# Optimization experiments

Hardware: AMD Instinct MI355X
Metric: run time of the kernel (lower is better)

The kernel has to match this reference:

```python
import jax, jax.numpy as jnp
import numpy as np

B, T, V, H = 256, 2048, 128, 64  # batch, seq_len, vocab/input_size, hidden_size


def setup_inputs() -> dict:
    key = jax.random.key(0)
    ks = jax.random.split(key, 11)
    s = 0.1  # weight scale
    d = jnp.float32
    return {
        "x": jax.random.normal(ks[0], (B, T, V), dtype=d),
        "W_f": jax.random.normal(ks[1], (V + H, H), dtype=d) * s,
        "b_f": jax.random.normal(ks[2], (H,), dtype=d) * s,
        "W_if": jax.random.normal(ks[3], (V + H, H), dtype=d) * s,
        "b_if": jax.random.normal(ks[4], (H,), dtype=d) * s,
        "W_ic": jax.random.normal(ks[5], (V + H, H), dtype=d) * s,
        "b_ic": jax.random.normal(ks[6], (H,), dtype=d) * s,
        "W_o": jax.random.normal(ks[7], (V + H, H), dtype=d) * s,
        "b_o": jax.random.normal(ks[8], (H,), dtype=d) * s,
        "W_out": jax.random.normal(ks[9], (H, V), dtype=d) * s,
        "b_out": jax.random.normal(ks[10], (V,), dtype=d) * s,
    }


def reference(x, W_f, b_f, W_if, b_if, W_ic, b_ic, W_o, b_o, W_out, b_out):
    # Manual LSTM cell from the source, stepped over time with lax.scan.
    # Per step (faithful to forward()+getOut()):
    #   s = concat(x_t, h);  f = sigmoid(s@W_f+b_f);  c = c*f
    #   add = tanh(s@W_ic+b_ic); af = sigmoid(s@W_if+b_if); c = c + add*af
    #   o = sigmoid(s@W_o+b_o);  h = tanh(c)*o
    #   out = softmax(h@W_out+b_out)
    b, t = x.shape[0], x.shape[1]
    h0 = jnp.zeros((b, W_f.shape[1]), dtype=x.dtype)
    c0 = jnp.zeros_like(h0)

    def step(carry, x_t):
        h, c = carry
        s = jnp.concatenate([x_t, h], axis=1)          # [B, V+H]
        f = jax.nn.sigmoid(s @ W_f + b_f)
        add = jnp.tanh(s @ W_ic + b_ic)
        af = jax.nn.sigmoid(s @ W_if + b_if)
        c = c * f + add * af
        o = jax.nn.sigmoid(s @ W_o + b_o)
        h = jnp.tanh(c) * o
        out = jax.nn.softmax(h @ W_out + b_out, axis=-1)  # [B, V]
        return (h, c), out

    (_, _), outs = jax.lax.scan(step, (h0, c0), jnp.swapaxes(x, 0, 1))
    return jnp.swapaxes(outs, 0, 1)  # [B, T, V]
```

## Files before the change

### kernel.cpp

```cpp
#include <hip/hip_runtime.h>
#include <cstdint>
#include <cstddef>

#define BB 256
#define TT 2048
#define VV 128
#define HH 64

typedef __attribute__((ext_vector_type(8))) short short8;
typedef __attribute__((ext_vector_type(4))) float f32x4;
typedef __attribute__((ext_vector_type(2))) float f32x2;

__device__ __forceinline__ float frcp(float x){ return __builtin_amdgcn_rcpf(x); }
__device__ __forceinline__ float sigm(float x){ return frcp(1.f + __expf(-x)); }
__device__ __forceinline__ float tanh_f(float x){ return 1.f - 2.f*frcp(1.f + __expf(2.f*x)); }

__device__ __forceinline__ void bar_lds(){
  asm volatile("s_waitcnt lgkmcnt(0)" ::: "memory");
  __builtin_amdgcn_s_barrier();
  __builtin_amdgcn_sched_barrier(0);
}

__device__ __forceinline__ void gload16(const void* g, void* l){
  __builtin_amdgcn_global_load_lds(
      (const __attribute__((address_space(1))) void*)g,
      (__attribute__((address_space(3))) void*)l, 16, 0, 0);
}

__device__ __forceinline__ unsigned short bf16hi(float x){
  unsigned u = __float_as_uint(x);
  return (unsigned short)((u + 0x7fffu + ((u>>16)&1u)) >> 16);
}
__device__ __forceinline__ void splitpack(const float* v8, short8& hi, short8& lo){
  #pragma unroll
  for (int j=0;j<8;++j){
    unsigned short h = bf16hi(v8[j]);
    float fh = __uint_as_float(((unsigned)h)<<16);
    unsigned short lw = bf16hi(v8[j] - fh);
    hi[j] = (short)h; lo[j] = (short)lw;
  }
}

__device__ __forceinline__ float qsum(float v){
  int t1 = __builtin_amdgcn_update_dpp(0, __float_as_int(v), 0xB1, 0xF, 0xF, true);
  v += __int_as_float(t1);
  int t2 = __builtin_amdgcn_update_dpp(0, __float_as_int(v), 0x4E, 0xF, 0xF, true);
  v += __int_as_float(t2);
  return v;
}

__device__ __forceinline__ void pkfma(f32x2& acc, f32x2 a, f32x2 b){
  asm volatile("v_pk_fma_f32 %0, %1, %2, %0" : "+v"(acc) : "v"(a), "v"(b));
}

__global__ __launch_bounds__(256) void conv_w_k(
  const float* __restrict__ Wf, const float* __restrict__ Wi,
  const float* __restrict__ Wc, const float* __restrict__ Wo,
  const float* __restrict__ Wout,
  unsigned short* __restrict__ W4h, unsigned short* __restrict__ W4l,
  unsigned short* __restrict__ WOh, unsigned short* __restrict__ WOl)
{
  const int idx = blockIdx.x*256 + threadIdx.x;
  if (idx < 32768){
    const int j = idx&7, l=(idx>>3)&63, kk=(idx>>9)&3, nt=idx>>11;
    const int k = kk*32 + (l>>4)*8 + j;
    const int n = nt*16 + (l&15);
    const int g = n&3, colw = n>>2;
    const float* Ws = (g==0)?Wf:((g==1)?Wi:((g==2)?Wc:Wo));
    const float v = Ws[k*HH + colw];
    const unsigned short h = bf16hi(v);
    const float fh = __uint_as_float(((unsigned)h)<<16);
    W4h[idx] = h; W4l[idx] = bf16hi(v - fh);
  }
  if (idx < 8192){
    const int j = idx&7, l=(idx>>3)&63, kk=(idx>>9)&1, jt=idx>>10;
    const int k = kk*32 + (l>>4)*8 + j;
    const int jc = jt*16 + (l&15);
    const float v = Wout[k*VV + jc];
    const unsigned short h = bf16hi(v);
    const float fh = __uint_as_float(((unsigned)h)<<16);
    WOh[idx] = h; WOl[idx] = bf16hi(v - fh);
  }
}

__global__ __launch_bounds__(512,1) void pre_gemm_k(
  const float* __restrict__ x, const unsigned short* __restrict__ W4h,
  const unsigned short* __restrict__ W4l, float* __restrict__ PRE)
{
  __shared__ __align__(16) unsigned short XFh[16384];
  __shared__ __align__(16) unsigned short XFl[16384];
  const int tid = threadIdx.x, wv = tid>>6, l = tid&63, b = blockIdx.x;

  short8 Bh[2][4], Bl[2][4];
  #pragma unroll
  for (int ntl=0; ntl<2; ++ntl){
    const int nt = wv*2 + ntl;
    #pragma unroll
    for (int kk=0; kk<4; ++kk){
      Bh[ntl][kk] = *(const short8*)(W4h + ((nt*4+kk)*64 + l)*8);
      Bl[ntl][kk] = *(const short8*)(W4l + ((nt*4+kk)*64 + l)*8);
    }
  }

  #pragma unroll 1
  for (int mt=0; mt<16; ++mt){
    const size_t base_row = (size_t)b*TT + mt*128;
    #pragma unroll
    for (int i=0;i<4;++i){
      const int G = tid*4+i;
      const int lf = G&63, kk=(G>>6)&3, m8=G>>8;
      const float* src = x + (base_row + m8*16 + (lf&15))*VV + kk*32 + (lf>>4)*8;
      const f32x4 u = *(const f32x4*)src;
      const f32x4 v = *(const f32x4*)(src+4);
      float tmp[8] = {u[0],u[1],u[2],u[3], v[0],v[1],v[2],v[3]};
      short8 hi, lo; splitpack(tmp, hi, lo);
      *(short8*)&XFh[(size_t)G*8] = hi;
      *(short8*)&XFl[(size_t)G*8] = lo;
    }
    bar_lds();
    for (int m8=0; m8<8; ++m8){
      short8 Ah[4], Al[4];
      #pragma unroll
      for (int kk=0;kk<4;++kk){
        Ah[kk] = *(const short8*)&XFh[((m8*4+kk)*64 + l)*8];
        Al[kk] = *(const short8*)&XFl[((m8*4+kk)*64 + l)*8];
      }
      #pragma unroll
      for (int ntl=0; ntl<2; ++ntl){
        f32x4 acc = {0.f,0.f,0.f,0.f};
        #pragma unroll
        for (int kk=0;kk<4;++kk){
          acc = __builtin_amdgcn_mfma_f32_16x16x32_bf16(Al[kk], Bh[ntl][kk], acc, 0,0,0);
          acc = __builtin_amdgcn_mfma_f32_16x16x32_bf16(Ah[kk], Bl[ntl][kk], acc, 0,0,0);
          acc = __builtin_amdgcn_mfma_f32_16x16x32_bf16(Ah[kk], Bh[ntl][kk], acc, 0,0,0);
        }
        const int nt = wv*2 + ntl;
        float* dst = PRE + (base_row + m8*16 + (l>>4)*4)*256 + nt*16 + (l&15);
        #pragma unroll
        for (int r=0;r<4;++r) dst[(size_t)r*256] = acc[r];
      }
    }
    bar_lds();
  }
}

__global__ __launch_bounds__(256,1) void recur_k(
  const float* __restrict__ W_f, const float* __restrict__ b_f,
  const float* __restrict__ W_if, const float* __restrict__ b_if,
  const float* __restrict__ W_ic, const float* __restrict__ b_ic,
  const float* __restrict__ W_o,  const float* __restrict__ b_o,
  const float* __restrict__ PRE,  float* __restrict__ H)
{
  __shared__ __align__(16) float ring[16*256];
  __shared__ __align__(16) float hring[32*HH];
  const int tid=threadIdx.x, wv=tid>>6, l=tid&63, b=blockIdx.x;
  const int col = wv*16 + (l>>2), q = l&3;

  f32x2 wf2[8], wi2[8], wc2[8], wo2[8];
  #pragma unroll
  for (int m=0;m<8;++m){
    const size_t k0 = (size_t)(VV + q*16 + 2*m)*HH + col;
    wf2[m] = f32x2{W_f [k0], W_f [k0+HH]};
    wi2[m] = f32x2{W_if[k0], W_if[k0+HH]};
    wc2[m] = f32x2{W_ic[k0], W_ic[k0+HH]};
    wo2[m] = f32x2{W_o [k0], W_o [k0+HH]};
  }
  const float b0=b_f[col], b1=b_if[col], b2=b_ic[col], b3=b_o[col];
  const float* PREb = PRE + (size_t)b*TT*256;
  float* Hb = H + (size_t)b*TT*HH;
  if (tid < HH) hring[31*HH + tid] = 0.f;

  if (wv==0){
    asm volatile("s_waitcnt vmcnt(0)" ::: "memory");
    #pragma unroll 1
    for (int s=0;s<15;++s) gload16(PREb + s*256 + l*4, &ring[s*256]);
    asm volatile("s_waitcnt vmcnt(14)" ::: "memory");
  }
  bar_lds();

  float c_ = 0.f;
  #pragma unroll 1
  for (int t=0;t<TT;++t){
    if (wv==1 && t>0 && (t&15)==0){
      #pragma unroll
      for (int i=0;i<4;++i){
        const int rt = t-16 + i*4 + (l>>4);
        const f32x4 v = *(const f32x4*)&hring[(rt&31)*HH + (l&15)*4];
        *(f32x4*)(Hb + (size_t)rt*HH + (l&15)*4) = v;
      }
    }
    const int rprev = (t+31)&31;
    const float* hb = &hring[rprev*HH + q*16];
    const f32x4 hv4[4] = { *(const f32x4*)(hb+0), *(const f32x4*)(hb+4),
                           *(const f32x4*)(hb+8), *(const f32x4*)(hb+12) };
    const f32x4 pre = *(const f32x4*)&ring[(t&15)*256 + col*4];
    f32x2 a0={0.f,0.f}, a1={0.f,0.f}, a2={0.f,0.f}, a3={0.f,0.f};
    #pragma unroll
    for (int m=0;m<4;++m){
      #pragma unroll
      for (int p=0;p<2;++p){
        const f32x2 hp = f32x2{hv4[m][2*p], hv4[m][2*p+1]};
        const int idx = m*2+p;
        pkfma(a0, hp, wf2[idx]);
        pkfma(a1, hp, wi2[idx]);
        pkfma(a2, hp, wc2[idx]);
        pkfma(a3, hp, wo2[idx]);
      }
    }
    const float d0 = qsum(a0[0]+a0[1]);
    const float d1 = qsum(a1[0]+a1[1]);
    const float d2 = qsum(a2[0]+a2[1]);
    const float d3 = qsum(a3[0]+a3[1]);
    const float f  = sigm (d0 + pre[0] + b0);
    const float fi = sigm (d1 + pre[1] + b1);
    const float ci = tanh_f(d2 + pre[2] + b2);
    const float o  = sigm (d3 + pre[3] + b3);
    c_ = c_*f + ci*fi;
    const float hv = tanh_f(c_) * o;
    if (q==0) hring[(t&31)*HH + col] = hv;
    if (wv==0){
      gload16(PREb + (size_t)((t+15)&(TT-1))*256 + l*4, &ring[((t+15)&15)*256]);
      asm volatile("s_waitcnt vmcnt(14)" ::: "memory");
    }
    bar_lds();
  }
  if (wv==1){
    #pragma unroll
    for (int i=0;i<4;++i){
      const int rt = TT-16 + i*4 + (l>>4);
      const f32x4 v = *(const f32x4*)&hring[(rt&31)*HH + (l&15)*4];
      *(f32x4*)(Hb + (size_t)rt*HH + (l&15)*4) = v;
    }
  }
}

__global__ __launch_bounds__(512,1) void logit_k(
  const float* __restrict__ H, const unsigned short* __restrict__ WOh,
  const unsigned short* __restrict__ WOl, const float* __restrict__ b_out,
  float* __restrict__ out)
{
  const int tid=threadIdx.x, wv=tid>>6, l=tid&63, b=blockIdx.x;
  short8 Bh[8][2], Bl[8][2];
  #pragma unroll
  for (int jt=0;jt<8;++jt){
    #pragma unroll
    for (int kk=0;kk<2;++kk){
      Bh[jt][kk] = *(const short8*)(WOh + ((jt*2+kk)*64 + l)*8);
      Bl[jt][kk] = *(const short8*)(WOl + ((jt*2+kk)*64 + l)*8);
    }
  }
  float bj[8];
  #pragma unroll
  for (int jt=0;jt<8;++jt) bj[jt] = b_out[jt*16 + (l&15)];

  #pragma unroll 1
  for (int mt=0; mt<16; ++mt){
    const size_t row0 = (size_t)b*TT + mt*128 + wv*16;
    const float* hbase = H + (row0 + (l&15))*HH;
    short8 Ah[2], Al[2];
    #pragma unroll
    for (int kk=0;kk<2;++kk){
      const float* s = hbase + kk*32 + (l>>4)*8;
      const f32x4 u = *(const f32x4*)s;
      const f32x4 v = *(const f32x4*)(s+4);
      float tmp[8] = {u[0],u[1],u[2],u[3], v[0],v[1],v[2],v[3]};
      splitpack(tmp, Ah[kk], Al[kk]);
    }
    f32x4 acc[8];
    #pragma unroll
    for (int jt=0;jt<8;++jt){
      f32x4 a = {0.f,0.f,0.f,0.f};
      #pragma unroll
      for (int kk=0;kk<2;++kk){
        a = __builtin_amdgcn_mfma_f32_16x16x32_bf16(Al[kk], Bh[jt][kk], a, 0,0,0);
        a = __builtin_amdgcn_mfma_f32_16x16x32_bf16(Ah[kk], Bl[jt][kk], a, 0,0,0);
        a = __builtin_amdgcn_mfma_f32_16x16x32_bf16(Ah[kk], Bh[jt][kk], a, 0,0,0);
      }
      acc[jt] = a;
    }
    #pragma unroll
    for (int r=0;r<4;++r){
      float z[8];
      #pragma unroll
      for (int jt=0;jt<8;++jt) z[jt] = acc[jt][r] + bj[jt];
      float mx = z[0];
      #pragma unroll
      for (int jt=1;jt<8;++jt) mx = fmaxf(mx, z[jt]);
      mx = fmaxf(mx, __shfl_xor(mx,1));
      mx = fmaxf(mx, __shfl_xor(mx,2));
      mx = fmaxf(mx, __shfl_xor(mx,4));
      mx = fmaxf(mx, __shfl_xor(mx,8));
      float sum = 0.f;
      #pragma unroll
      for (int jt=0;jt<8;++jt){ z[jt] = __expf(z[jt]-mx); sum += z[jt]; }
      sum += __shfl_xor(sum,1);
      sum += __shfl_xor(sum,2);
      sum += __shfl_xor(sum,4);
      sum += __shfl_xor(sum,8);
      const float rs = frcp(sum);
      float* op = out + (row0 + (l>>4)*4 + r)*VV + (l&15);
      #pragma unroll
      for (int jt=0;jt<8;++jt) op[jt*16] = z[jt]*rs;
    }
  }
}

#define XA_IDX(buf,kk,q,s) ((buf)*2048 + (((kk)*4+(q))*16+(s))*8)
#define HA_IDX(buf,kk,q,s) ((buf)*1024 + (((kk)*4+(q))*16+(s))*8)
#define NBF 128

__device__ __forceinline__ void gload16f(const float* g, float* l){
  __builtin_amdgcn_global_load_lds(
      (const __attribute__((address_space(1))) void*)g,
      (__attribute__((address_space(3))) void*)l, 16, 0, 0);
}

__global__ __launch_bounds__(512, 1) void fused_fb_k(
  const float* __restrict__ x,
  const float* __restrict__ W_f,  const float* __restrict__ b_f,
  const float* __restrict__ W_if, const float* __restrict__ b_if,
  const float* __restrict__ W_ic, const float* __restrict__ b_ic,
  const float* __restrict__ W_o,  const float* __restrict__ b_o,
  const float* __restrict__ W_out,const float* __restrict__ b_out,
  float* __restrict__ out)
{
  __shared__ __align__(16) float XR[4*16*VV];
  __shared__ __align__(16) short XAh[2*2048];
  __shared__ __align__(16) short XAl[2*2048];
  __shared__ __align__(16) float PRE[32*256];
  __shared__ __align__(16) short HAh[2*1024];
  __shared__ __align__(16) short HAl[2*1024];
  __shared__ __align__(16) float HR[32*HH];

  const int tid = threadIdx.x;
  const int wv  = tid >> 6;
  const int l   = tid & 63;
  const int row = blockIdx.x;
  const float* xrow = x   + (size_t)row*TT*VV;
  float*       orow = out + (size_t)row*TT*VV;

  if (wv < 4) {
    const int col = (wv&3)*16 + (l>>2);
    const int q   = l&3;
    float wh0[16], wh1[16], wh2[16], wh3[16];
    #pragma unroll
    for (int m=0;m<16;++m){
      const size_t kidx = (size_t)(VV + q*16 + m)*HH + col;
      wh0[m]=W_f[kidx]; wh1[m]=W_if[kidx]; wh2[m]=W_ic[kidx]; wh3[m]=W_o[kidx];
    }
    const float b0=b_f[col], b1=b_if[col], b2=b_ic[col], b3=b_o[col];
    if (tid < HH) HR[31*HH + tid] = 0.f;
    bar_lds(); bar_lds(); bar_lds();
    float c = 0.f;
    #pragma unroll 1
    for (int t=0; t<TT; ++t){
      const f32x4* hp = (const f32x4*)&HR[((t+31)&31)*HH + q*16];
      const f32x4 pre4 = *(const f32x4*)&PRE[(t&31)*256 + col*4];
      float d0=0.f,d1=0.f,d2=0.f,d3=0.f;
      #pragma unroll
      for (int m=0;m<4;++m){
        const f32x4 hv = hp[m];
        #pragma unroll
        for (int e=0;e<4;++e){
          const float s = hv[e];
          d0 = fmaf(s, wh0[m*4+e], d0);
          d1 = fmaf(s, wh1[m*4+e], d1);
          d2 = fmaf(s, wh2[m*4+e], d2);
          d3 = fmaf(s, wh3[m*4+e], d3);
        }
      }
      d0 = qsum(d0); d1 = qsum(d1); d2 = qsum(d2); d3 = qsum(d3);
      const float f  = sigm(d0 + pre4[0] + b0);
      const float fi = sigm(d1 + pre4[1] + b1);
      const float ci = tanh_f(d2 + pre4[2] + b2);
      const float o  = sigm(d3 + pre4[3] + b3);
      c = c*f + ci*fi;
      const float hv2 = tanh_f(c) * o;
      if (q==0) HR[(t&31)*HH + col] = hv2;
      bar_lds();
    }
    bar_lds();
  } else {
    const int pv = wv - 4;
    const int pt = pv*64 + l;
    short8 Bh[4][4], Bl[4][4];
    #pragma unroll
    for (int ntl=0; ntl<4; ++ntl){
      const int n = (pv*4+ntl)*16 + (l&15);
      const int g = n&3, colw = n>>2;
      const float* Ws = (g==0)?W_f:((g==1)?W_if:((g==2)?W_ic:W_o));
      #pragma unroll
      for (int kk=0;kk<4;++kk){
        float tmp[8];
        #pragma unroll
        for (int j=0;j<8;++j) tmp[j] = Ws[(size_t)(kk*32+(l>>4)*8+j)*HH + colw];
        splitpack(tmp, Bh[ntl][kk], Bl[ntl][kk]);
      }
    }
    short8 Lh[2][2], Ll[2][2];
    #pragma unroll
    for (int jt=0; jt<2; ++jt){
      const int j = (pv*2+jt)*16 + (l&15);
      #pragma unroll
      for (int kk=0;kk<2;++kk){
        float tmp[8];
        #pragma unroll
        for (int jj=0;jj<8;++jj) tmp[jj] = W_out[(size_t)(kk*32+(l>>4)*8+jj)*VV + j];
        splitpack(tmp, Lh[jt][kk], Ll[jt][kk]);
      }
    }
    auto GLOAD = [&](int bb){
      #pragma unroll
      for (int i=0;i<2;++i){
        const float* src = xrow + (size_t)bb*16*VV + pv*512 + i*256 + l*4;
        float* dst = &XR[(bb&3)*2048 + pv*512 + i*256];
        gload16f(src, dst);
      }
    };
    auto CONV = [&](int bb){
      if (pt < 256){
        const int buf=bb&1, kk=pt>>6, qq=(pt>>4)&3, s=pt&15;
        const float* src = &XR[(bb&3)*2048 + s*VV + kk*32 + qq*8];
        float tmp[8];
        #pragma unroll
        for (int j=0;j<8;++j) tmp[j] = src[j];
        short8 hi, lo; splitpack(tmp, hi, lo);
        *(short8*)&XAh[XA_IDX(buf,kk,qq,s)] = hi;
        *(short8*)&XAl[XA_IDX(buf,kk,qq,s)] = lo;
      }
    };
    auto PREB = [&](int bb){
      const int buf = bb&1;
      short8 Ah[4], Al[4];
      #pragma unroll
      for (int kk=0;kk<4;++kk){
        Ah[kk] = *(const short8*)&XAh[XA_IDX(buf,kk,(l>>4),(l&15))];
        Al[kk] = *(const short8*)&XAl[XA_IDX(buf,kk,(l>>4),(l&15))];
      }
      #pragma unroll
      for (int ntl=0; ntl<4; ++ntl){
        f32x4 acc = {0.f,0.f,0.f,0.f};
        #pragma unroll
        for (int kk=0;kk<4;++kk){
          acc = __builtin_amdgcn_mfma_f32_16x16x32_bf16(Al[kk], Bh[ntl][kk], acc, 0,0,0);
          acc = __builtin_amdgcn_mfma_f32_16x16x32_bf16(Ah[kk], Bl[ntl][kk], acc, 0,0,0);
          acc = __builtin_amdgcn_mfma_f32_16x16x32_bf16(Ah[kk], Bh[ntl][kk], acc, 0,0,0);
        }
        const int n  = (pv*4+ntl)*16 + (l&15);
        const int s0 = buf*16 + (l>>4)*4;
        #pragma unroll
        for (int r=0;r<4;++r) PRE[(s0+r)*256 + n] = acc[r];
      }
    };
    auto LOGB = [&](int bb){
      const int buf = bb&1;
      short8 Ah[2], Al[2];
      #pragma unroll
      for (int kk=0;kk<2;++kk){
        Ah[kk] = *(const short8*)&HAh[HA_IDX(buf,kk,(l>>4),(l&15))];
        Al[kk] = *(const short8*)&HAl[HA_IDX(buf,kk,(l>>4),(l&15))];
      }
      #pragma unroll
      for (int jt=0; jt<2; ++jt){
        f32x4 acc = {0.f,0.f,0.f,0.f};
        #pragma unroll
        for (int kk=0;kk<2;++kk){
          acc = __builtin_amdgcn_mfma_f32_16x16x32_bf16(Al[kk], Lh[jt][kk], acc, 0,0,0);
          acc = __builtin_amdgcn_mfma_f32_16x16x32_bf16(Ah[kk], Ll[jt][kk], acc, 0,0,0);
          acc = __builtin_amdgcn_mfma_f32_16x16x32_bf16(Ah[kk], Lh[jt][kk], acc, 0,0,0);
        }
        const int j  = (pv*2+jt)*16 + (l&15);
        const int t0 = bb*16 + (l>>4)*4;
        #pragma unroll
        for (int r=0;r<4;++r) orow[(size_t)(t0+r)*VV + j] = acc[r];
      }
    };
    auto RELAY = [&](int hs){
      if (pt < 8){
        const int kk = pt>>2, qq = pt&3;
        const int buf = (hs>>4)&1, s = hs&15;
        const float* src = &HR[(hs&31)*HH + kk*32 + qq*8];
        float tmp[8];
        #pragma unroll
        for (int j=0;j<8;++j) tmp[j] = src[j];
        short8 hi, lo; splitpack(tmp, hi, lo);
        *(short8*)&HAh[HA_IDX(buf,kk,qq,s)] = hi;
        *(short8*)&HAl[HA_IDX(buf,kk,qq,s)] = lo;
      }
    };
    GLOAD(0); GLOAD(1); GLOAD(2);
    asm volatile("s_waitcnt vmcnt(2)" ::: "memory");
    bar_lds();
    CONV(0); CONV(1);
    bar_lds();
    PREB(0);
    bar_lds();
    #pragma unroll 1
    for (int t=0; t<TT; ++t){
      if (t >= 1) RELAY(t-1);
      const int slot = t&15, blk = t>>4;
      if (slot==0){ if (blk+1 < NBF) PREB(blk+1); }
      else if (slot==1){ if (blk >= 1) LOGB(blk-1); }
      else if (slot==2){ if (blk+3 < NBF) GLOAD(blk+3); }
      else if (slot==3){ if (blk+2 < NBF) asm volatile("s_waitcnt vmcnt(2)" ::: "memory"); }
      else if (slot==4){ if (blk+2 < NBF) CONV(blk+2); }
      bar_lds();
    }
    RELAY(TT-1);
    bar_lds();
    LOGB(NBF-1);
  }
}

__global__ __launch_bounds__(256) void softmax_fb_k(float* __restrict__ out)
{
  const int r = blockIdx.x*4 + (threadIdx.x>>6);
  const int l = threadIdx.x & 63;
  float2* p = (float2*)(out + (size_t)r*VV);
  float2 v = p[l];
  float m = fmaxf(v.x, v.y);
  #pragma unroll
  for (int d=1; d<64; d<<=1) m = fmaxf(m, __shfl_xor(m, d));
  float e0 = __expf(v.x - m), e1 = __expf(v.y - m);
  float s = e0 + e1;
  #pragma unroll
  for (int d=1; d<64; d<<=1) s += __shfl_xor(s, d);
  float rs = frcp(s);
  p[l] = make_float2(e0*rs, e1*rs);
}

extern "C" void kernel_launch(void* const* d_in, const int* in_sizes, int n_in,
                              void* d_out, int out_size, void* d_ws, size_t ws_size,
                              hipStream_t stream) {
  const float* x     = (const float*)d_in[0];
  const float* W_f   = (const float*)d_in[1];
  const float* b_f   = (const float*)d_in[2];
  const float* W_if  = (const float*)d_in[3];
  const float* b_if  = (const float*)d_in[4];
  const float* W_ic  = (const float*)d_in[5];
  const float* b_ic  = (const float*)d_in[6];
  const float* W_o   = (const float*)d_in[7];
  const float* b_o   = (const float*)d_in[8];
  const float* W_out = (const float*)d_in[9];
  const float* b_out = (const float*)d_in[10];
  float* out = (float*)d_out;

  const size_t PRE_B = (size_t)BB*TT*256*sizeof(float);
  const size_t H_B   = (size_t)BB*TT*HH*sizeof(float);
  const size_t need  = PRE_B + H_B + 2*32768*2 + 2*8192*2;

  if (ws_size >= need) {
    char* w = (char*)d_ws;
    float* PRE  = (float*)w;
    float* Hbuf = (float*)(w + PRE_B);
    unsigned short* W4h = (unsigned short*)(w + PRE_B + H_B);
    unsigned short* W4l = W4h + 32768;
    unsigned short* WOh = W4l + 32768;
    unsigned short* WOl = WOh + 8192;
    hipLaunchKernelGGL(conv_w_k, dim3(128), dim3(256), 0, stream,
                       W_f, W_if, W_ic, W_o, W_out, W4h, W4l, WOh, WOl);
    hipLaunchKernelGGL(pre_gemm_k, dim3(BB), dim3(512), 0, stream, x, W4h, W4l, PRE);
    hipLaunchKernelGGL(recur_k, dim3(BB), dim3(256), 0, stream,
                       W_f, b_f, W_if, b_if, W_ic, b_ic, W_o, b_o, PRE, Hbuf);
    hipLaunchKernelGGL(logit_k, dim3(BB), dim3(512), 0, stream, Hbuf, WOh, WOl, b_out, out);
  } else {
    hipLaunchKernelGGL(fused_fb_k, dim3(BB), dim3(512), 0, stream,
                       x, W_f, b_f, W_if, b_if, W_ic, b_ic, W_o, b_o,
                       W_out, b_out, out);
    hipLaunchKernelGGL(softmax_fb_k, dim3(BB*TT/4), dim3(256), 0, stream, out);
  }
}
```

Before: 1.004 ms.

## Split recurrent dot products over eight lanes with 512-thread recurrence blocks

The recurrence kernel now runs with 8 waves instead of 4. Each hidden column's 64-element dot product is split across 8 lanes (8 k-values each) rather than 4 lanes (16 each), which halves the serial FMA chain per step. The cross-lane reduction gains a third stage through ds_swizzle. The serial per-timestep latency should drop, at the cost of more waves synchronising at every step's barrier and an extra swizzle on the critical path.

Measured after the change: 1.178 ms. 1.17x slower.

```diff
diff --git a/kernel.cpp b/kernel.cpp
--- a/kernel.cpp
+++ b/kernel.cpp
@@ -46,6 +46,16 @@
   v += __int_as_float(t1);
   int t2 = __builtin_amdgcn_update_dpp(0, __float_as_int(v), 0x4E, 0xF, 0xF, true);
   v += __int_as_float(t2);
+  return v;
+}
+
+__device__ __forceinline__ float osum(float v){
+  int t1 = __builtin_amdgcn_update_dpp(0, __float_as_int(v), 0xB1, 0xF, 0xF, true);
+  v += __int_as_float(t1);
+  int t2 = __builtin_amdgcn_update_dpp(0, __float_as_int(v), 0x4E, 0xF, 0xF, true);
+  v += __int_as_float(t2);
+  int t3 = __builtin_amdgcn_ds_swizzle(__float_as_int(v), 0x101F);
+  v += __int_as_float(t3);
   return v;
 }
 
@@ -144,7 +154,7 @@
   }
 }
 
-__global__ __launch_bounds__(256,1) void recur_k(
+__global__ __launch_bounds__(512,1) void recur3_k(
   const float* __restrict__ W_f, const float* __restrict__ b_f,
   const float* __restrict__ W_if, const float* __restrict__ b_if,
   const float* __restrict__ W_ic, const float* __restrict__ b_ic,
@@ -154,20 +164,24 @@
   __shared__ __align__(16) float ring[16*256];
   __shared__ __align__(16) float hring[32*HH];
   const int tid=threadIdx.x, wv=tid>>6, l=tid&63, b=blockIdx.x;
-  const int col = wv*16 + (l>>2), q = l&3;
-
-  f32x2 wf2[8], wi2[8], wc2[8], wo2[8];
-  #pragma unroll
-  for (int m=0;m<8;++m){
-    const size_t k0 = (size_t)(VV + q*16 + 2*m)*HH + col;
-    wf2[m] = f32x2{W_f [k0], W_f [k0+HH]};
-    wi2[m] = f32x2{W_if[k0], W_if[k0+HH]};
-    wc2[m] = f32x2{W_ic[k0], W_ic[k0+HH]};
-    wo2[m] = f32x2{W_o [k0], W_o [k0+HH]};
+  const int col = wv*8 + (l>>3);
+  const int ks  = l&7;
+
+  f32x2 wf[4], wi[4], wc[4], wo[4];
+  #pragma unroll
+  for (int m=0;m<4;++m){
+    const size_t k0 = (size_t)(VV + ks*8 + 2*m)*HH + col;
+    wf[m] = f32x2{W_f [k0], W_f [k0+HH]};
+    wi[m] = f32x2{W_if[k0], W_if[k0+HH]};
+    wc[m] = f32x2{W_ic[k0], W_ic[k0+HH]};
+    wo[m] = f32x2{W_o [k0], W_o [k0+HH]};
   }
   const float b0=b_f[col], b1=b_if[col], b2=b_ic[col], b3=b_o[col];
   const float* PREb = PRE + (size_t)b*TT*256;
   float* Hb = H + (size_t)b*TT*HH;
+  const f32x4* ring4  = (const f32x4*)ring;
+  const f32x4* hring4 = (const f32x4*)hring;
+
   if (tid < HH) hring[31*HH + tid] = 0.f;
 
   if (wv==0){
@@ -185,39 +199,32 @@
       #pragma unroll
       for (int i=0;i<4;++i){
         const int rt = t-16 + i*4 + (l>>4);
-        const f32x4 v = *(const f32x4*)&hring[(rt&31)*HH + (l&15)*4];
+        const f32x4 v = hring4[(rt&31)*16 + (l&15)];
         *(f32x4*)(Hb + (size_t)rt*HH + (l&15)*4) = v;
       }
     }
     const int rprev = (t+31)&31;
-    const float* hb = &hring[rprev*HH + q*16];
-    const f32x4 hv4[4] = { *(const f32x4*)(hb+0), *(const f32x4*)(hb+4),
-                           *(const f32x4*)(hb+8), *(const f32x4*)(hb+12) };
-    const f32x4 pre = *(const f32x4*)&ring[(t&15)*256 + col*4];
+    const f32x4 ha = hring4[rprev*16 + ks*2];
+    const f32x4 hb = hring4[rprev*16 + ks*2 + 1];
+    const f32x4 pre = ring4[(t&15)*64 + col];
     f32x2 a0={0.f,0.f}, a1={0.f,0.f}, a2={0.f,0.f}, a3={0.f,0.f};
-    #pragma unroll
-    for (int m=0;m<4;++m){
-      #pragma unroll
-      for (int p=0;p<2;++p){
-        const f32x2 hp = f32x2{hv4[m][2*p], hv4[m][2*p+1]};
-        const int idx = m*2+p;
-        pkfma(a0, hp, wf2[idx]);
-        pkfma(a1, hp, wi2[idx]);
-        pkfma(a2, hp, wc2[idx]);
-        pkfma(a3, hp, wo2[idx]);
-      }
-    }
-    const float d0 = qsum(a0[0]+a0[1]);
-    const float d1 = qsum(a1[0]+a1[1]);
-    const float d2 = qsum(a2[0]+a2[1]);
-    const float d3 = qsum(a3[0]+a3[1]);
+    const f32x2 p0 = f32x2{ha[0],ha[1]}, p1 = f32x2{ha[2],ha[3]};
+    const f32x2 p2 = f32x2{hb[0],hb[1]}, p3 = f32x2{hb[2],hb[3]};
+    pkfma(a0,p0,wf[0]); pkfma(a0,p1,wf[1]); pkfma(a0,p2,wf[2]); pkfma(a0,p3,wf[3]);
+    pkfma(a1,p0,wi[0]); pkfma(a1,p1,wi[1]); pkfma(a1,p2,wi[2]); pkfma(a1,p3,wi[3]);
+    pkfma(a2,p0,wc[0]); pkfma(a2,p1,wc[1]); pkfma(a2,p2,wc[2]); pkfma(a2,p3,wc[3]);
+    pkfma(a3,p0,wo[0]); pkfma(a3,p1,wo[1]); pkfma(a3,p2,wo[2]); pkfma(a3,p3,wo[3]);
+    const float d0 = osum(a0[0]+a0[1]);
+    const float d1 = osum(a1[0]+a1[1]);
+    const float d2 = osum(a2[0]+a2[1]);
+    const float d3 = osum(a3[0]+a3[1]);
     const float f  = sigm (d0 + pre[0] + b0);
     const float fi = sigm (d1 + pre[1] + b1);
     const float ci = tanh_f(d2 + pre[2] + b2);
     const float o  = sigm (d3 + pre[3] + b3);
     c_ = c_*f + ci*fi;
     const float hv = tanh_f(c_) * o;
-    if (q==0) hring[(t&31)*HH + col] = hv;
+    if (ks==0) hring[(t&31)*HH + col] = hv;
     if (wv==0){
       gload16(PREb + (size_t)((t+15)&(TT-1))*256 + l*4, &ring[((t+15)&15)*256]);
       asm volatile("s_waitcnt vmcnt(14)" ::: "memory");
@@ -228,7 +235,7 @@
     #pragma unroll
     for (int i=0;i<4;++i){
       const int rt = TT-16 + i*4 + (l>>4);
-      const f32x4 v = *(const f32x4*)&hring[(rt&31)*HH + (l&15)*4];
+      const f32x4 v = hring4[(rt&31)*16 + (l&15)];
       *(f32x4*)(Hb + (size_t)rt*HH + (l&15)*4) = v;
     }
   }
@@ -475,11 +482,11 @@
         for (int r=0;r<4;++r) orow[(size_t)(t0+r)*VV + j] = acc[r];
       }
     };
-    auto RELAY = [&](int hs){
+    auto RELAY = [&](int hs2){
       if (pt < 8){
         const int kk = pt>>2, qq = pt&3;
-        const int buf = (hs>>4)&1, s = hs&15;
-        const float* src = &HR[(hs&31)*HH + kk*32 + qq*8];
+        const int buf = (hs2>>4)&1, s = hs2&15;
+        const float* src = &HR[(hs2&31)*HH + kk*32 + qq*8];
         float tmp[8];
         #pragma unroll
         for (int j=0;j<8;++j) tmp[j] = src[j];
@@ -560,7 +567,7 @@
     hipLaunchKernelGGL(conv_w_k, dim3(128), dim3(256), 0, stream,
                        W_f, W_if, W_ic, W_o, W_out, W4h, W4l, WOh, WOl);
     hipLaunchKernelGGL(pre_gemm_k, dim3(BB), dim3(512), 0, stream, x, W4h, W4l, PRE);
-    hipLaunchKernelGGL(recur_k, dim3(BB), dim3(256), 0, stream,
+    hipLaunchKernelGGL(recur3_k, dim3(BB), dim3(512), 0, stream,
                        W_f, b_f, W_if, b_if, W_ic, b_ic, W_o, b_o, PRE, Hbuf);
     hipLaunchKernelGGL(logit_k, dim3(BB), dim3(512), 0, stream, Hbuf, WOh, WOl, b_out, out);
   } else {
```
